# Kernel tuning notes

Hardware: AMD Instinct MI355X
Metric: run time of the kernel (lower is better)

The kernel has to match this reference:

```python
import jax, jax.numpy as jnp
import numpy as np

B, N, C, H, I, ID = 4, 1024, 1024, 16, 77, 768
HD = C // H
HID = 4 * C


def _ln(t, w, b):
    m = jnp.mean(t, axis=-1, keepdims=True)
    v = jnp.mean((t - m) ** 2, axis=-1, keepdims=True)
    return (t - m) * jax.lax.rsqrt(v + 1e-5) * w + b


def _gelu(t):
    return jax.nn.gelu(t, approximate=False)


def setup_inputs() -> dict:
    key = jax.random.key(0)
    ks = iter(jax.random.split(key, 16))

    def nrm(shape, s=0.02):
        return jax.random.normal(next(ks), shape, jnp.float32) * s

    return {
        'x': jax.random.normal(next(ks), (B, N, C), jnp.float32),
        'instruct_states': jax.random.normal(next(ks), (B, I, ID), jnp.float32),
        'norm1_w': jnp.ones((C,), jnp.float32), 'norm1_b': jnp.zeros((C,), jnp.float32),
        'qkv_w': nrm((3 * C, C)),
        'q_bias': jnp.zeros((C,), jnp.float32), 'v_bias': jnp.zeros((C,), jnp.float32),
        'proj_w': nrm((C, C)), 'proj_b': jnp.zeros((C,), jnp.float32),
        'gamma_1': jnp.full((C,), 1e-5, jnp.float32), 'gamma_2': jnp.full((C,), 1e-5, jnp.float32),
        'norm2_w': jnp.ones((C,), jnp.float32), 'norm2_b': jnp.zeros((C,), jnp.float32),
        'fc1_w': nrm((HID, C)), 'fc1_b': jnp.zeros((HID,), jnp.float32),
        'fc2_w': nrm((C, HID)), 'fc2_b': jnp.zeros((C,), jnp.float32),
        'pfc1_w': nrm((HID, C)), 'pfc1_b': jnp.zeros((HID,), jnp.float32),
        'pfc2_w': nrm((C, HID)), 'pfc2_b': jnp.zeros((C,), jnp.float32),
        'parallel_gate': jnp.full((1,), 0.1, jnp.float32),
        'ir_ln_w': jnp.ones((ID,), jnp.float32), 'ir_ln_b': jnp.zeros((ID,), jnp.float32),
        'ir_l1_w': nrm((C, ID)), 'ir_l1_b': jnp.zeros((C,), jnp.float32),
        'ir_l2_w': nrm((C, C)), 'ir_l2_b': jnp.zeros((C,), jnp.float32),
    }


def reference(x, instruct_states, norm1_w, norm1_b, qkv_w, q_bias, v_bias,
              proj_w, proj_b, gamma_1, gamma_2, norm2_w, norm2_b,
              fc1_w, fc1_b, fc2_w, fc2_b, pfc1_w, pfc1_b, pfc2_w, pfc2_b,
              parallel_gate, ir_ln_w, ir_ln_b, ir_l1_w, ir_l1_b, ir_l2_w, ir_l2_b):
    # instruct_dim_reduce: LN -> Linear -> GELU -> Linear
    kv = _ln(instruct_states, ir_ln_w, ir_ln_b)
    kv = _gelu(kv @ ir_l1_w.T + ir_l1_b) @ ir_l2_w.T + ir_l2_b  # [B, I, C]

    xn = _ln(x, norm1_w, norm1_b)                               # [B, N, C]
    cat = jnp.concatenate([kv, xn], axis=1)                     # [B, I+N, C]
    S = I + N

    qkv_bias = jnp.concatenate([q_bias, jnp.zeros_like(v_bias), v_bias])
    qkv = (cat @ qkv_w.T + qkv_bias).reshape(B, S, 3, H, HD)
    q = qkv[:, :, 0].transpose(0, 2, 1, 3)                      # [B, H, S, HD]
    k = qkv[:, :, 1].transpose(0, 2, 1, 3)
    v = qkv[:, :, 2].transpose(0, 2, 1, 3)

    # only visual queries, keys/values over instructions + visual tokens
    q = q[:, :, I:, :] * (HD ** -0.5)                           # [B, H, N, HD]
    attn = jnp.einsum('bhqd,bhkd->bhqk', q, k)                  # [B, H, N, S]
    attn = jax.nn.softmax(attn, axis=-1)
    o = jnp.einsum('bhqk,bhkd->bqhd', attn, v).reshape(B, N, C)
    o = o @ proj_w.T + proj_b

    x = x + gamma_1 * o                                         # LayerScale residual

    y = _ln(x, norm2_w, norm2_b)
    mlp = _gelu(y @ fc1_w.T + fc1_b) @ fc2_w.T + fc2_b
    pmlp = _gelu(y @ pfc1_w.T + pfc1_b) @ pfc2_w.T + pfc2_b
    x = x + gamma_2 * mlp + parallel_gate * pmlp
    return x
```

## Files before the change

kernel.cpp:

```cpp
#include <hip/hip_runtime.h>
#include <cstdint>

#define Bv   4
#define Nv   1024
#define Cv   1024
#define Hv   16
#define Iv   77
#define IDv  768
#define HDv  64
#define HIDv 4096
#define Sv   (Iv + Nv)
#define BIv  (Bv * Iv)
#define BSv  (Bv * Sv)
#define BNv  (Bv * Nv)
#define SPADv 1152

typedef __bf16 bf16x8_t __attribute__((ext_vector_type(8)));
typedef float  f32x4_t  __attribute__((ext_vector_type(4)));
typedef unsigned short us8_t __attribute__((ext_vector_type(8)));
typedef long  l2_t  __attribute__((ext_vector_type(2)));

__device__ inline f32x4_t zero4() { f32x4_t z; z[0]=0.f; z[1]=0.f; z[2]=0.f; z[3]=0.f; return z; }

__device__ inline unsigned short f2bf(float f) {
    unsigned int u = __builtin_bit_cast(unsigned int, f);
    u = (u + 0x7fffu + ((u >> 16) & 1u)) >> 16;
    return (unsigned short)u;
}
__device__ inline float bf2f(unsigned short u) {
    return __builtin_bit_cast(float, ((unsigned int)u) << 16);
}
__device__ inline unsigned int f4_fp8(float a, float b, float c, float d) {
    int v = __builtin_amdgcn_cvt_pk_fp8_f32(a, b, 0, false);
    v = __builtin_amdgcn_cvt_pk_fp8_f32(c, d, v, true);
    return (unsigned int)v;
}

__device__ inline float gelu_f(float x) {
    float u = 0.7978845608f * x * (1.0f + 0.044715f * x * x);
    float e = __expf(2.0f * u);
    float t = 1.0f - 2.0f / (e + 1.0f);
    return 0.5f * x * (1.0f + t);
}

__device__ inline void gload_lds16(const void* g, void* l) {
    __builtin_amdgcn_global_load_lds(
        (__attribute__((address_space(1))) void*)(unsigned long long)g,
        (__attribute__((address_space(3))) void*)(unsigned long long)l,
        16, 0, 0);
}

__global__ __launch_bounds__(256) void cvt8_kernel(
        const float* s0, const float* s1, const float* s2, const float* s3,
        const float* s4, const float* s5, const float* s6, const float* s7,
        void* d0, void* d1, void* d2, void* d3,
        void* d4, void* d5, void* d6, void* d7,
        const float* g1, const float* g2, const float* gate) {
    long i = (long)blockIdx.x * 256 + threadIdx.x;
    const float* src; void* dst; long off;
    const float* sptr = nullptr; int K4 = 1; float wmul = 1.0f; bool f8 = false;
    if (i < 2097152) {
        if (i < 786432)       { src = s0; dst = d0; off = i; }
        else if (i < 1048576) { src = s1; dst = d1; off = i - 786432;  sptr = g1; K4 = 256; }
        else                  { src = s2; dst = d2; off = i - 1048576; f8 = true; wmul = 32.f; }
    } else if (i < 4194304) {
        if (i < 3145728)      { src = s3; dst = d3; off = i - 2097152; f8 = true; wmul = 32.f; sptr = g2; K4 = 1024; }
        else                  { src = s4; dst = d4; off = i - 3145728; f8 = true; wmul = 32.f; }
    } else {
        if (i < 5242880)      { src = s5; dst = d5; off = i - 4194304; f8 = true; wmul = 32.f; sptr = gate; K4 = 0x7fffffff; }
        else if (i < 5439488) { src = s6; dst = d6; off = i - 5242880; }
        else                  { src = s7; dst = d7; off = i - 5439488; }
    }
    float sc = (sptr ? sptr[(int)(off / K4)] : 1.0f) * wmul;
    float4 v = ((const float4*)src)[off];
    if (f8) {
        ((unsigned int*)dst)[off] = f4_fp8(v.x * sc, v.y * sc, v.z * sc, v.w * sc);
    } else {
        ushort4 o = {f2bf(v.x * sc), f2bf(v.y * sc), f2bf(v.z * sc), f2bf(v.w * sc)};
        ((ushort4*)dst)[off] = o;
    }
}

__global__ __launch_bounds__(256) void bias_prep_kernel(
        const float* __restrict__ qb, const float* __restrict__ vb,
        const float* __restrict__ fc2b, const float* __restrict__ pfc2b,
        const float* __restrict__ projb_in,
        const float* __restrict__ fc1b, const float* __restrict__ pfc1b,
        const float* __restrict__ g1, const float* __restrict__ g2,
        const float* __restrict__ gate,
        float* __restrict__ qkvb, float* __restrict__ bfuse,
        float* __restrict__ projb, float* __restrict__ bcat) {
    int i = blockIdx.x * 256 + threadIdx.x;
    if (i < 3 * Cv) {
        float v = 0.f;
        if (i < Cv) v = qb[i];
        else if (i >= 2 * Cv) v = vb[i - 2 * Cv];
        qkvb[i] = v;
    } else if (i < 4 * Cv) {
        int n = i - 3 * Cv;
        bfuse[n] = g2[n] * fc2b[n] + gate[0] * pfc2b[n];
    } else if (i < 5 * Cv) {
        int n = i - 4 * Cv;
        projb[n] = g1[n] * projb_in[n];
    } else if (i < 13 * Cv) {
        int j = i - 5 * Cv;
        bcat[j] = (j < HIDv) ? fc1b[j] : pfc1b[j - HIDv];
    }
}

__global__ __launch_bounds__(256) void scatter_kv_kernel(const unsigned short* __restrict__ kv,
                                                         unsigned short* __restrict__ cat) {
    int r = blockIdx.x;
    int b = r / Iv, i = r % Iv;
    const uint2* src = (const uint2*)(kv + (size_t)r * Cv);
    uint2* dst = (uint2*)(cat + (size_t)(b * Sv + i) * Cv);
    dst[threadIdx.x] = src[threadIdx.x];
}

template <int F8>
__global__ __launch_bounds__(256) void ln_kernel(const float* __restrict__ in,
                                                 const float* __restrict__ w,
                                                 const float* __restrict__ bvec,
                                                 void* __restrict__ out,
                                                 int cols, float invcols,
                                                 int div_, int stride_, int off_) {
    const int r = blockIdx.x;
    const int tid = threadIdx.x;
    const float* row = in + (size_t)r * cols;
    float s = 0.f, s2 = 0.f;
    for (int c = tid * 4; c < cols; c += 1024) {
        float4 v = *(const float4*)(row + c);
        s  += v.x + v.y + v.z + v.w;
        s2 += v.x * v.x + v.y * v.y + v.z * v.z + v.w * v.w;
    }
#pragma unroll
    for (int o2 = 32; o2 > 0; o2 >>= 1) { s += __shfl_down(s, o2); s2 += __shfl_down(s2, o2); }
    __shared__ float sh[10];
    const int lane = tid & 63, wave = tid >> 6;
    if (lane == 0) { sh[wave] = s; sh[4 + wave] = s2; }
    __syncthreads();
    if (tid == 0) {
        float S1 = sh[0] + sh[1] + sh[2] + sh[3];
        float S2 = sh[4] + sh[5] + sh[6] + sh[7];
        float mean = S1 * invcols;
        float var  = S2 * invcols - mean * mean;
        sh[8] = mean;
        sh[9] = rsqrtf(var + 1e-5f);
    }
    __syncthreads();
    const float mean = sh[8], rstd = sh[9];
    const size_t orow = (size_t)((r / div_) * stride_ + (r % div_) + off_) * cols;
    for (int c = tid * 4; c < cols; c += 1024) {
        float4 v  = *(const float4*)(row + c);
        float4 wv = *(const float4*)(w + c);
        float4 bv = *(const float4*)(bvec + c);
        float o0 = (v.x - mean) * rstd * wv.x + bv.x;
        float o1 = (v.y - mean) * rstd * wv.y + bv.y;
        float o2 = (v.z - mean) * rstd * wv.z + bv.z;
        float o3 = (v.w - mean) * rstd * wv.w + bv.w;
        if constexpr (F8) {
            *(unsigned int*)((unsigned char*)out + orow + c) =
                f4_fp8(o0 * 16.f, o1 * 16.f, o2 * 16.f, o3 * 16.f);
        } else {
            ushort4 o = {f2bf(o0), f2bf(o1), f2bf(o2), f2bf(o3)};
            *(ushort4*)((unsigned short*)out + orow + c) = o;
        }
    }
}

template <int MODE>
__global__ __launch_bounds__(256) void gemm_bf16_kernel(
        const unsigned short* __restrict__ A,
        const unsigned short* __restrict__ W,
        const float* __restrict__ bias,
        unsigned short* __restrict__ outp,
        int M, int N, int K) {
    __shared__ unsigned short As[2][128 * 32];
    __shared__ unsigned short Bs[2][128 * 32];
    const int tid  = threadIdx.x;
    const int lane = tid & 63;
    const int wave = tid >> 6;
    const int m16  = lane & 15;
    const int g4   = lane >> 4;
    const int n0 = blockIdx.x * 128;
    const int m0 = blockIdx.y * 128;
    const int wm = (wave >> 1) * 64;
    const int wn = (wave & 1) * 64;

    const int r0  = tid >> 2;
    const int cc0 = (tid & 3) * 8;
    int am0 = m0 + r0;       if (am0 > M - 1) am0 = M - 1;
    int am1 = m0 + r0 + 64;  if (am1 > M - 1) am1 = M - 1;
    const unsigned short* agp0 = A + (size_t)am0 * K + cc0;
    const unsigned short* agp1 = A + (size_t)am1 * K + cc0;
    const unsigned short* bgp0 = W + (size_t)(n0 + r0) * K + cc0;
    const unsigned short* bgp1 = W + (size_t)(n0 + r0 + 64) * K + cc0;

    f32x4_t acc[4][4];
#pragma unroll
    for (int a = 0; a < 4; ++a)
#pragma unroll
        for (int bb = 0; bb < 4; ++bb) acc[a][bb] = zero4();

    auto stage = [&](int buf) {
        gload_lds16(agp0, &As[buf][wave * 512]);
        gload_lds16(agp1, &As[buf][2048 + wave * 512]);
        gload_lds16(bgp0, &Bs[buf][wave * 512]);
        gload_lds16(bgp1, &Bs[buf][2048 + wave * 512]);
        agp0 += 32; agp1 += 32; bgp0 += 32; bgp1 += 32;
    };

    stage(0);
    const int NIT = K >> 5;
    for (int it = 0; it < NIT; ++it) {
        const int cur = it & 1;
        __syncthreads();
        if (it + 1 < NIT) stage(cur ^ 1);
        bf16x8_t xf[4], wf[4];
#pragma unroll
        for (int bb = 0; bb < 4; ++bb)
            xf[bb] = *(const bf16x8_t*)&As[cur][(wm + bb * 16 + m16) * 32 + g4 * 8];
#pragma unroll
        for (int a = 0; a < 4; ++a)
            wf[a] = *(const bf16x8_t*)&Bs[cur][(wn + a * 16 + m16) * 32 + g4 * 8];
#pragma unroll
        for (int a = 0; a < 4; ++a)
#pragma unroll
            for (int bb = 0; bb < 4; ++bb)
                acc[a][bb] = __builtin_amdgcn_mfma_f32_16x16x32_bf16(wf[a], xf[bb], acc[a][bb], 0, 0, 0);
    }

#pragma unroll
    for (int a = 0; a < 4; ++a) {
        const int cb = n0 + wn + a * 16 + g4 * 4;
        const float4 bv4 = *(const float4*)(bias + cb);
#pragma unroll
        for (int bb = 0; bb < 4; ++bb) {
            const int r = m0 + wm + bb * 16 + m16;
            if (r < M) {
                const size_t idx = (size_t)r * N + cb;
                const float v0 = acc[a][bb][0] + bv4.x;
                const float v1 = acc[a][bb][1] + bv4.y;
                const float v2 = acc[a][bb][2] + bv4.z;
                const float v3 = acc[a][bb][3] + bv4.w;
                if constexpr (MODE == 0) {
                    ushort4 o = {f2bf(v0), f2bf(v1), f2bf(v2), f2bf(v3)};
                    *(ushort4*)(outp + idx) = o;
                } else {
                    ushort4 o = {f2bf(gelu_f(v0)), f2bf(gelu_f(v1)),
                                 f2bf(gelu_f(v2)), f2bf(gelu_f(v3))};
                    *(ushort4*)(outp + idx) = o;
                }
            }
        }
    }
}

__global__ __launch_bounds__(256) void gemm_splitk_kernel(
        const unsigned short* __restrict__ A1,
        const unsigned short* __restrict__ W1,
        unsigned short* __restrict__ parts,
        int M, int N, int KA, int Kc) {
    __shared__ unsigned short As[2][128 * 32];
    __shared__ unsigned short Bs[2][128 * 32];
    const int tid  = threadIdx.x;
    const int lane = tid & 63;
    const int wave = tid >> 6;
    const int m16  = lane & 15;
    const int g4   = lane >> 4;
    const int bid = blockIdx.x;
    const int xcd = bid & 7, l = bid >> 3;
    const int by = (xcd << 2) | (l & 3);
    const int rr = l >> 2;
    const int bx = rr & 7;
    const int z  = rr >> 3;
    const int n0 = bx * 128;
    const int m0 = by * 128;
    const int wm = (wave >> 1) * 64;
    const int wn = (wave & 1) * 64;
    const int k0 = z * Kc;

    const int r0  = tid >> 2;
    const int cc0 = (tid & 3) * 8;
    const unsigned short* agp0 = A1 + (size_t)(m0 + r0) * KA + k0 + cc0;
    const unsigned short* agp1 = A1 + (size_t)(m0 + r0 + 64) * KA + k0 + cc0;
    const unsigned short* bgp0 = W1 + (size_t)(n0 + r0) * KA + k0 + cc0;
    const unsigned short* bgp1 = W1 + (size_t)(n0 + r0 + 64) * KA + k0 + cc0;

    f32x4_t acc[4][4];
#pragma unroll
    for (int a = 0; a < 4; ++a)
#pragma unroll
        for (int bb = 0; bb < 4; ++bb) acc[a][bb] = zero4();

    auto stage = [&](int buf) {
        gload_lds16(agp0, &As[buf][wave * 512]);
        gload_lds16(agp1, &As[buf][2048 + wave * 512]);
        gload_lds16(bgp0, &Bs[buf][wave * 512]);
        gload_lds16(bgp1, &Bs[buf][2048 + wave * 512]);
        agp0 += 32; agp1 += 32; bgp0 += 32; bgp1 += 32;
    };

    stage(0);
    const int NIT = Kc >> 5;
    for (int it = 0; it < NIT; ++it) {
        const int cur = it & 1;
        __syncthreads();
        if (it + 1 < NIT) stage(cur ^ 1);
        bf16x8_t xf[4], wf[4];
#pragma unroll
        for (int bb = 0; bb < 4; ++bb)
            xf[bb] = *(const bf16x8_t*)&As[cur][(wm + bb * 16 + m16) * 32 + g4 * 8];
#pragma unroll
        for (int a = 0; a < 4; ++a)
            wf[a] = *(const bf16x8_t*)&Bs[cur][(wn + a * 16 + m16) * 32 + g4 * 8];
#pragma unroll
        for (int a = 0; a < 4; ++a)
#pragma unroll
            for (int bb = 0; bb < 4; ++bb)
                acc[a][bb] = __builtin_amdgcn_mfma_f32_16x16x32_bf16(wf[a], xf[bb], acc[a][bb], 0, 0, 0);
    }

    unsigned short* pz = parts + (size_t)z * M * N;
#pragma unroll
    for (int a = 0; a < 4; ++a) {
        const int cb = n0 + wn + a * 16 + g4 * 4;
#pragma unroll
        for (int bb = 0; bb < 4; ++bb) {
            const int r = m0 + wm + bb * 16 + m16;
            const size_t idx = (size_t)r * N + cb;
            ushort4 o = {f2bf(acc[a][bb][0]), f2bf(acc[a][bb][1]),
                         f2bf(acc[a][bb][2]), f2bf(acc[a][bb][3])};
            *(ushort4*)(pz + idx) = o;
        }
    }
}

__global__ __launch_bounds__(256) void gemm_fp8_gelu_kernel(
        const unsigned char* __restrict__ A,
        const unsigned char* __restrict__ W,
        const float* __restrict__ bias,
        unsigned char* __restrict__ outp,
        int M, int N, int K) {
    __shared__ unsigned char As[2][128 * 64];
    __shared__ unsigned char Bs[2][128 * 64];
    const int tid  = threadIdx.x;
    const int lane = tid & 63;
    const int wave = tid >> 6;
    const int m16  = lane & 15;
    const int g4   = lane >> 4;
    const int bid = blockIdx.x;
    const int xcd = bid & 7, l = bid >> 3;
    const int by = (xcd << 2) | (l & 3);
    const int bx = l >> 2;
    const int n0 = bx * 128;
    const int m0 = by * 128;
    const int wm = (wave >> 1) * 64;
    const int wn = (wave & 1) * 64;

    const int r0  = tid >> 2;
    const int cc0 = (tid & 3) * 16;
    const unsigned char* agp0 = A + (size_t)(m0 + r0) * K + cc0;
    const unsigned char* agp1 = A + (size_t)(m0 + r0 + 64) * K + cc0;
    const unsigned char* bgp0 = W + (size_t)(n0 + r0) * K + cc0;
    const unsigned char* bgp1 = W + (size_t)(n0 + r0 + 64) * K + cc0;

    f32x4_t acc[4][4];
#pragma unroll
    for (int a = 0; a < 4; ++a)
#pragma unroll
        for (int bb = 0; bb < 4; ++bb) acc[a][bb] = zero4();

    auto stage = [&](int buf) {
        gload_lds16(agp0, &As[buf][wave * 1024]);
        gload_lds16(agp1, &As[buf][4096 + wave * 1024]);
        gload_lds16(bgp0, &Bs[buf][wave * 1024]);
        gload_lds16(bgp1, &Bs[buf][4096 + wave * 1024]);
        agp0 += 64; agp1 += 64; bgp0 += 64; bgp1 += 64;
    };

    stage(0);
    const int NIT = K >> 6;
    for (int it = 0; it < NIT; ++it) {
        const int cur = it & 1;
        __syncthreads();
        if (it + 1 < NIT) stage(cur ^ 1);
        l2_t xv[4], wv[4];
#pragma unroll
        for (int bb = 0; bb < 4; ++bb)
            xv[bb] = *(const l2_t*)&As[cur][(wm + bb * 16 + m16) * 64 + g4 * 16];
#pragma unroll
        for (int a = 0; a < 4; ++a)
            wv[a] = *(const l2_t*)&Bs[cur][(wn + a * 16 + m16) * 64 + g4 * 16];
#pragma unroll
        for (int a = 0; a < 4; ++a)
#pragma unroll
            for (int bb = 0; bb < 4; ++bb) {
                acc[a][bb] = __builtin_amdgcn_mfma_f32_16x16x32_fp8_fp8(wv[a][0], xv[bb][0], acc[a][bb], 0, 0, 0);
                acc[a][bb] = __builtin_amdgcn_mfma_f32_16x16x32_fp8_fp8(wv[a][1], xv[bb][1], acc[a][bb], 0, 0, 0);
            }
    }

    const float ds = 1.0f / 512.0f;
#pragma unroll
    for (int a = 0; a < 4; ++a) {
        const int cb = n0 + wn + a * 16 + g4 * 4;
        const float4 bv4 = *(const float4*)(bias + cb);
#pragma unroll
        for (int bb = 0; bb < 4; ++bb) {
            const int r = m0 + wm + bb * 16 + m16;
            const size_t idx = (size_t)r * N + cb;
            unsigned int pk = f4_fp8(gelu_f(acc[a][bb][0] * ds + bv4.x) * 16.f,
                                     gelu_f(acc[a][bb][1] * ds + bv4.y) * 16.f,
                                     gelu_f(acc[a][bb][2] * ds + bv4.z) * 16.f,
                                     gelu_f(acc[a][bb][3] * ds + bv4.w) * 16.f);
            *(unsigned int*)(outp + idx) = pk;
        }
    }
}

__global__ __launch_bounds__(256) void gemm_fp8_splitk_kernel(
        const unsigned char* __restrict__ A1,
        const unsigned char* __restrict__ W1,
        const unsigned char* __restrict__ A2,
        const unsigned char* __restrict__ W2,
        unsigned short* __restrict__ parts,
        int M, int N, int lda, int ldw, int Kc, int zsplit) {
    __shared__ unsigned char As[2][128 * 64];
    __shared__ unsigned char Bs[2][128 * 64];
    const int tid  = threadIdx.x;
    const int lane = tid & 63;
    const int wave = tid >> 6;
    const int m16  = lane & 15;
    const int g4   = lane >> 4;
    const int bid = blockIdx.x;
    const int xcd = bid & 7, l = bid >> 3;
    const int by = (xcd << 2) | (l & 3);
    const int rr = l >> 2;
    const int bx = rr & 7;
    const int z  = rr >> 3;
    const int n0 = bx * 128;
    const int m0 = by * 128;
    const int wm = (wave >> 1) * 64;
    const int wn = (wave & 1) * 64;

    const unsigned char* A = (z < zsplit) ? A1 : A2;
    const unsigned char* W = (z < zsplit) ? W1 : W2;
    const int k0 = (z % zsplit) * Kc;

    const int r0  = tid >> 2;
    const int cc0 = (tid & 3) * 16;
    const unsigned char* agp0 = A + (size_t)(m0 + r0) * lda + k0 + cc0;
    const unsigned char* agp1 = A + (size_t)(m0 + r0 + 64) * lda + k0 + cc0;
    const unsigned char* bgp0 = W + (size_t)(n0 + r0) * ldw + k0 + cc0;
    const unsigned char* bgp1 = W + (size_t)(n0 + r0 + 64) * ldw + k0 + cc0;

    f32x4_t acc[4][4];
#pragma unroll
    for (int a = 0; a < 4; ++a)
#pragma unroll
        for (int bb = 0; bb < 4; ++bb) acc[a][bb] = zero4();

    auto stage = [&](int buf) {
        gload_lds16(agp0, &As[buf][wave * 1024]);
        gload_lds16(agp1, &As[buf][4096 + wave * 1024]);
        gload_lds16(bgp0, &Bs[buf][wave * 1024]);
        gload_lds16(bgp1, &Bs[buf][4096 + wave * 1024]);
        agp0 += 64; agp1 += 64; bgp0 += 64; bgp1 += 64;
    };

    stage(0);
    const int NIT = Kc >> 6;
    for (int it = 0; it < NIT; ++it) {
        const int cur = it & 1;
        __syncthreads();
        if (it + 1 < NIT) stage(cur ^ 1);
        l2_t xv[4], wv[4];
#pragma unroll
        for (int bb = 0; bb < 4; ++bb)
            xv[bb] = *(const l2_t*)&As[cur][(wm + bb * 16 + m16) * 64 + g4 * 16];
#pragma unroll
        for (int a = 0; a < 4; ++a)
            wv[a] = *(const l2_t*)&Bs[cur][(wn + a * 16 + m16) * 64 + g4 * 16];
#pragma unroll
        for (int a = 0; a < 4; ++a)
#pragma unroll
            for (int bb = 0; bb < 4; ++bb) {
                acc[a][bb] = __builtin_amdgcn_mfma_f32_16x16x32_fp8_fp8(wv[a][0], xv[bb][0], acc[a][bb], 0, 0, 0);
                acc[a][bb] = __builtin_amdgcn_mfma_f32_16x16x32_fp8_fp8(wv[a][1], xv[bb][1], acc[a][bb], 0, 0, 0);
            }
    }

    unsigned short* pz = parts + (size_t)z * M * N;
    const float ds = 1.0f / 512.0f;
#pragma unroll
    for (int a = 0; a < 4; ++a) {
        const int cb = n0 + wn + a * 16 + g4 * 4;
#pragma unroll
        for (int bb = 0; bb < 4; ++bb) {
            const int r = m0 + wm + bb * 16 + m16;
            const size_t idx = (size_t)r * N + cb;
            ushort4 o = {f2bf(acc[a][bb][0] * ds), f2bf(acc[a][bb][1] * ds),
                         f2bf(acc[a][bb][2] * ds), f2bf(acc[a][bb][3] * ds)};
            *(ushort4*)(pz + idx) = o;
        }
    }
}

template <int NP>
__global__ __launch_bounds__(256) void reduce_kernel(
        const unsigned short* __restrict__ parts,
        const float* __restrict__ resid,
        const float* __restrict__ bias,
        float* __restrict__ out, int MN, int N4mask) {
    int i = blockIdx.x * 256 + threadIdx.x;
    if (i * 4 >= MN) return;
    float4 res = ((const float4*)resid)[i];
    float4 bv  = *(const float4*)(bias + (i & N4mask) * 4);
    float4 o = {res.x + bv.x, res.y + bv.y, res.z + bv.z, res.w + bv.w};
#pragma unroll
    for (int z = 0; z < NP; ++z) {
        ushort4 u = ((const ushort4*)(parts + (size_t)z * MN))[i];
        o.x += bf2f(u.x); o.y += bf2f(u.y); o.z += bf2f(u.z); o.w += bf2f(u.w);
    }
    ((float4*)out)[i] = o;
}

__global__ __launch_bounds__(256) void vtrans_kernel(const unsigned short* __restrict__ qkv,
                                                     unsigned short* __restrict__ vt) {
    __shared__ unsigned short Vs[64 * 64];
    const int stile = blockIdx.x;
    const int bh = blockIdx.y;
    const int b = bh >> 4, h = bh & 15;
    const int tid = threadIdx.x;
#pragma unroll
    for (int j = 0; j < 2; ++j) {
        int c = j * 256 + tid;
        int r = c >> 3, d8 = (c & 7) * 8;
        int s = stile * 64 + r;
        uint4 v = {0u, 0u, 0u, 0u};
        if (s < Sv) v = *(const uint4*)(qkv + ((size_t)(b * Sv + s) * 3 + 2) * Cv + h * 64 + d8);
        *(uint4*)&Vs[r * 64 + d8] = v;
    }
    __syncthreads();
    const int d  = tid >> 2;
    const int p0 = (tid & 3) * 16;
    unsigned short tmp[16];
#pragma unroll
    for (int e = 0; e < 16; ++e) {
        int p = p0 + e;
        int s_local = (p & 32) + 16 * ((p >> 2) & 1) + 4 * ((p & 31) >> 3) + (p & 3);
        tmp[e] = Vs[s_local * 64 + d];
    }
    unsigned short* dst = vt + ((size_t)bh * 64 + d) * SPADv + stile * 64 + p0;
    *(uint4*)dst       = *(const uint4*)&tmp[0];
    *(uint4*)(dst + 8) = *(const uint4*)&tmp[8];
}

__global__ __launch_bounds__(256) void attn_kernel(const unsigned short* __restrict__ qkv,
                                                   const unsigned short* __restrict__ vt,
                                                   unsigned short* __restrict__ o) {
    __shared__ unsigned short Qs[64 * 64];
    __shared__ unsigned short Ks[2][64 * 64];
    __shared__ unsigned short Vts[2][64 * 64];

    const int tid  = threadIdx.x;
    const int lane = tid & 63;
    const int wave = tid >> 6;
    const int m16  = lane & 15;
    const int g4   = lane >> 4;
    const int qt = blockIdx.x;
    const int bh = blockIdx.y;
    const int b = bh >> 4, h = bh & 15;

    const int lr = lane >> 3;
    const int csw = ((lane & 7) ^ lr) * 8;
    const int sw7 = m16 & 7;

#pragma unroll
    for (int j = 0; j < 2; ++j) {
        int r = wave * 16 + j * 8 + lr;
        int s = Iv + qt * 64 + r;
        gload_lds16(qkv + ((size_t)(b * Sv + s) * 3) * Cv + h * 64 + csw,
                    &Qs[(wave * 16 + j * 8) * 64]);
    }

    auto stage_kv = [&](int st, int buf) {
#pragma unroll
        for (int j = 0; j < 2; ++j) {
            int r = wave * 16 + j * 8 + lr;
            int s = st * 64 + r; if (s > Sv - 1) s = Sv - 1;
            gload_lds16(qkv + ((size_t)(b * Sv + s) * 3 + 1) * Cv + h * 64 + csw,
                        &Ks[buf][(wave * 16 + j * 8) * 64]);
            gload_lds16(vt + ((size_t)bh * 64 + r) * SPADv + st * 64 + csw,
                        &Vts[buf][(wave * 16 + j * 8) * 64]);
        }
    };

    f32x4_t oacc[4];
#pragma unroll
    for (int dt = 0; dt < 4; ++dt) oacc[dt] = zero4();
    float m_run = -1e30f, l_run = 0.f;

    stage_kv(0, 0);
    __syncthreads();

    const bf16x8_t qf0 = *(const bf16x8_t*)&Qs[(wave * 16 + m16) * 64 + ((g4 ^ sw7) * 8)];
    const bf16x8_t qf1 = *(const bf16x8_t*)&Qs[(wave * 16 + m16) * 64 + (((4 + g4) ^ sw7) * 8)];

    const int NT = (Sv + 63) / 64;
    for (int st = 0; st < NT; ++st) {
        const int cur = st & 1;
        if (st + 1 < NT) stage_kv(st + 1, cur ^ 1);

        f32x4_t sc[4];
#pragma unroll
        for (int kt = 0; kt < 4; ++kt) {
            bf16x8_t k0 = *(const bf16x8_t*)&Ks[cur][(kt * 16 + m16) * 64 + ((g4 ^ sw7) * 8)];
            bf16x8_t k1 = *(const bf16x8_t*)&Ks[cur][(kt * 16 + m16) * 64 + (((4 + g4) ^ sw7) * 8)];
            f32x4_t z = zero4();
            z = __builtin_amdgcn_mfma_f32_16x16x32_bf16(k0, qf0, z, 0, 0, 0);
            z = __builtin_amdgcn_mfma_f32_16x16x32_bf16(k1, qf1, z, 0, 0, 0);
            sc[kt] = z;
        }

        float mx = -1e30f;
#pragma unroll
        for (int kt = 0; kt < 4; ++kt)
#pragma unroll
            for (int r = 0; r < 4; ++r) {
                int key = st * 64 + kt * 16 + g4 * 4 + r;
                float v = sc[kt][r] * 0.125f;
                v = (key < Sv) ? v : -1e30f;
                sc[kt][r] = v;
                mx = fmaxf(mx, v);
            }
        mx = fmaxf(mx, __shfl_xor(mx, 16));
        mx = fmaxf(mx, __shfl_xor(mx, 32));
        const float mnew  = fmaxf(m_run, mx);
        const float alpha = __expf(m_run - mnew);
        m_run = mnew;
        float sum = 0.f;
#pragma unroll
        for (int kt = 0; kt < 4; ++kt)
#pragma unroll
            for (int r = 0; r < 4; ++r) {
                float p = __expf(sc[kt][r] - mnew);
                sc[kt][r] = p;
                sum += p;
            }
        sum += __shfl_xor(sum, 16);
        sum += __shfl_xor(sum, 32);
        l_run = l_run * alpha + sum;
#pragma unroll
        for (int dt = 0; dt < 4; ++dt) oacc[dt] *= alpha;

        us8_t pu0, pu1;
#pragma unroll
        for (int j = 0; j < 8; ++j) {
            pu0[j] = f2bf(sc[(j >> 2)][j & 3]);
            pu1[j] = f2bf(sc[2 + (j >> 2)][j & 3]);
        }
        const bf16x8_t pf0 = __builtin_bit_cast(bf16x8_t, pu0);
        const bf16x8_t pf1 = __builtin_bit_cast(bf16x8_t, pu1);

#pragma unroll
        for (int dt = 0; dt < 4; ++dt) {
            bf16x8_t v0 = *(const bf16x8_t*)&Vts[cur][(dt * 16 + m16) * 64 + ((g4 ^ sw7) * 8)];
            bf16x8_t v1 = *(const bf16x8_t*)&Vts[cur][(dt * 16 + m16) * 64 + (((4 + g4) ^ sw7) * 8)];
            oacc[dt] = __builtin_amdgcn_mfma_f32_16x16x32_bf16(v0, pf0, oacc[dt], 0, 0, 0);
            oacc[dt] = __builtin_amdgcn_mfma_f32_16x16x32_bf16(v1, pf1, oacc[dt], 0, 0, 0);
        }
        __syncthreads();
    }

    const float inv = 1.0f / l_run;
    const int q = qt * 64 + wave * 16 + m16;
    const size_t row = (size_t)(b * Nv + q) * Cv + h * 64;
#pragma unroll
    for (int dt = 0; dt < 4; ++dt) {
        ushort4 o4 = {f2bf(oacc[dt][0] * inv), f2bf(oacc[dt][1] * inv),
                      f2bf(oacc[dt][2] * inv), f2bf(oacc[dt][3] * inv)};
        *(ushort4*)&o[row + dt * 16 + g4 * 4] = o4;
    }
}

extern "C" void kernel_launch(void* const* d_in, const int* in_sizes, int n_in,
                              void* d_out, int out_size, void* d_ws, size_t ws_size,
                              hipStream_t stream) {
    (void)in_sizes; (void)n_in; (void)out_size; (void)ws_size;
    const float* x       = (const float*)d_in[0];
    const float* instr   = (const float*)d_in[1];
    const float* norm1_w = (const float*)d_in[2];
    const float* norm1_b = (const float*)d_in[3];
    const float* qkv_w   = (const float*)d_in[4];
    const float* q_bias  = (const float*)d_in[5];
    const float* v_bias  = (const float*)d_in[6];
    const float* proj_w  = (const float*)d_in[7];
    const float* proj_b  = (const float*)d_in[8];
    const float* gamma_1 = (const float*)d_in[9];
    const float* gamma_2 = (const float*)d_in[10];
    const float* norm2_w = (const float*)d_in[11];
    const float* norm2_b = (const float*)d_in[12];
    const float* fc1_w   = (const float*)d_in[13];
    const float* fc1_b   = (const float*)d_in[14];
    const float* fc2_w   = (const float*)d_in[15];
    const float* fc2_b   = (const float*)d_in[16];
    const float* pfc1_w  = (const float*)d_in[17];
    const float* pfc1_b  = (const float*)d_in[18];
    const float* pfc2_w  = (const float*)d_in[19];
    const float* pfc2_b  = (const float*)d_in[20];
    const float* gate    = (const float*)d_in[21];
    const float* ir_ln_w = (const float*)d_in[22];
    const float* ir_ln_b = (const float*)d_in[23];
    const float* ir_l1_w = (const float*)d_in[24];
    const float* ir_l1_b = (const float*)d_in[25];
    const float* ir_l2_w = (const float*)d_in[26];
    const float* ir_l2_b = (const float*)d_in[27];
    float* out = (float*)d_out;

    char* ws = (char*)d_ws;
    size_t off = 0;
    auto alloc = [&](size_t bytes) -> char* {
        char* p = ws + off;
        off += (bytes + 255) & ~(size_t)255;
        return p;
    };
    unsigned short* w_qkv  = (unsigned short*)alloc((size_t)3 * Cv * Cv * 2);
    unsigned short* w_proj = (unsigned short*)alloc((size_t)Cv * Cv * 2);
    unsigned char*  w_mlp1 = (unsigned char*)alloc((size_t)2 * HIDv * Cv);
    unsigned char*  w_fc2  = (unsigned char*)alloc((size_t)Cv * HIDv);
    unsigned char*  w_pfc2 = (unsigned char*)alloc((size_t)Cv * HIDv);
    unsigned short* w_ir1  = (unsigned short*)alloc((size_t)Cv * IDv * 2);
    unsigned short* w_ir2  = (unsigned short*)alloc((size_t)Cv * Cv * 2);
    float*          qkvb   = (float*)alloc((size_t)3 * Cv * 4);
    float*          bfuse  = (float*)alloc((size_t)Cv * 4);
    float*          projb  = (float*)alloc((size_t)Cv * 4);
    float*          bcat   = (float*)alloc((size_t)2 * HIDv * 4);
    unsigned short* irln   = (unsigned short*)alloc((size_t)BIv * IDv * 2);
    unsigned short* h1     = (unsigned short*)alloc((size_t)BIv * Cv * 2);
    unsigned short* kvtmp  = (unsigned short*)alloc((size_t)BIv * Cv * 2);
    unsigned short* cat    = (unsigned short*)alloc((size_t)BSv * Cv * 2);
    unsigned short* qkvbuf = (unsigned short*)alloc((size_t)BSv * 3 * Cv * 2);
    unsigned short* obuf   = (unsigned short*)alloc((size_t)BNv * Cv * 2);
    float*          x1     = (float*)alloc((size_t)BNv * Cv * 4);
    unsigned char*  ybuf8  = (unsigned char*)alloc((size_t)BNv * Cv);
    unsigned char*  gbufA  = (unsigned char*)alloc((size_t)BNv * 2 * HIDv);
    unsigned short* fpart  = (unsigned short*)alloc((size_t)4 * BNv * Cv * 2);
    unsigned short* vt     = (unsigned short*)gbufA;
    unsigned short* ppart  = cat;

    cvt8_kernel<<<22272, 256, 0, stream>>>(qkv_w, proj_w, fc1_w, fc2_w, pfc1_w, pfc2_w,
                                           ir_l1_w, ir_l2_w,
                                           w_qkv, w_proj, w_mlp1, w_fc2,
                                           w_mlp1 + (size_t)HIDv * Cv, w_pfc2,
                                           w_ir1, w_ir2,
                                           gamma_1, gamma_2, gate);

    bias_prep_kernel<<<52, 256, 0, stream>>>(q_bias, v_bias, fc2_b, pfc2_b, proj_b,
                                             fc1_b, pfc1_b,
                                             gamma_1, gamma_2, gate,
                                             qkvb, bfuse, projb, bcat);

    ln_kernel<0><<<BIv, 256, 0, stream>>>(instr, ir_ln_w, ir_ln_b, irln,
                                          IDv, 1.0f / IDv, 1 << 28, 0, 0);
    ln_kernel<0><<<BNv, 256, 0, stream>>>(x, norm1_w, norm1_b, cat,
                                          Cv, 1.0f / Cv, Nv, Sv, Iv);
    gemm_bf16_kernel<1><<<dim3(Cv / 128, (BIv + 127) / 128), 256, 0, stream>>>(
        irln, w_ir1, ir_l1_b, h1, BIv, Cv, IDv);
    gemm_bf16_kernel<0><<<dim3(Cv / 128, (BIv + 127) / 128), 256, 0, stream>>>(
        h1, w_ir2, ir_l2_b, kvtmp, BIv, Cv, Cv);
    scatter_kv_kernel<<<BIv, 256, 0, stream>>>(kvtmp, cat);

    gemm_bf16_kernel<0><<<dim3(3 * Cv / 128, (BSv + 127) / 128), 256, 0, stream>>>(
        cat, w_qkv, qkvb, qkvbuf, BSv, 3 * Cv, Cv);

    vtrans_kernel<<<dim3(18, Bv * Hv), 256, 0, stream>>>(qkvbuf, vt);
    attn_kernel<<<dim3(Nv / 64, Bv * Hv), 256, 0, stream>>>(qkvbuf, vt, obuf);

    gemm_splitk_kernel<<<1024, 256, 0, stream>>>(
        obuf, w_proj, ppart, BNv, Cv, Cv, Cv / 4);
    reduce_kernel<4><<<(BNv * Cv / 4 + 255) / 256, 256, 0, stream>>>(
        ppart, x, projb, x1, BNv * Cv, Cv / 4 - 1);

    ln_kernel<1><<<BNv, 256, 0, stream>>>(x1, norm2_w, norm2_b, ybuf8,
                                          Cv, 1.0f / Cv, 1 << 28, 0, 0);

    gemm_fp8_gelu_kernel<<<2048, 256, 0, stream>>>(
        ybuf8, w_mlp1, bcat, gbufA, BNv, 2 * HIDv, Cv);

    gemm_fp8_splitk_kernel<<<1024, 256, 0, stream>>>(
        gbufA, w_fc2, gbufA + HIDv, w_pfc2, fpart,
        BNv, Cv, 2 * HIDv, HIDv, HIDv / 2, 2);
    reduce_kernel<4><<<(BNv * Cv / 4 + 255) / 256, 256, 0, stream>>>(
        fpart, x1, bfuse, out, BNv * Cv, Cv / 4 - 1);
}
```

Baseline: 505.0 us.

## Use gfx950 16x16x128 scaled FP8 MFMA with K=128 tiles and swizzled LDS

Replaces the pairs of 16x16x32 FP8 MFMAs in the GELU and split-K FP8 GEMMs with the gfx950 16x16x128 f8f6f4 scaled MFMA, using unit scales. The K tile grows from 64 to 128 and LDS buffers double. An XOR swizzle on 16-byte slots keeps LDS fragment reads conflict-free. The aim is fewer MFMA issues and barriers per K step, at the cost of more LDS per block, which may reduce occupancy.

```diff
diff --git a/kernel.cpp b/kernel.cpp
--- a/kernel.cpp
+++ b/kernel.cpp
@@ -19,6 +19,8 @@
 typedef float  f32x4_t  __attribute__((ext_vector_type(4)));
 typedef unsigned short us8_t __attribute__((ext_vector_type(8)));
 typedef long  l2_t  __attribute__((ext_vector_type(2)));
+typedef int   i32x4_t __attribute__((ext_vector_type(4)));
+typedef int   i32x8_t __attribute__((ext_vector_type(8)));
 
 __device__ inline f32x4_t zero4() { f32x4_t z; z[0]=0.f; z[1]=0.f; z[2]=0.f; z[3]=0.f; return z; }
 
@@ -48,6 +50,15 @@
         (__attribute__((address_space(1))) void*)(unsigned long long)g,
         (__attribute__((address_space(3))) void*)(unsigned long long)l,
         16, 0, 0);
+}
+
+__device__ inline i32x8_t frag32(const unsigned char* p0, const unsigned char* p1) {
+    i32x4_t lo = *(const i32x4_t*)p0;
+    i32x4_t hi = *(const i32x4_t*)p1;
+    i32x8_t r;
+    r[0] = lo[0]; r[1] = lo[1]; r[2] = lo[2]; r[3] = lo[3];
+    r[4] = hi[0]; r[5] = hi[1]; r[6] = hi[2]; r[7] = hi[3];
+    return r;
 }
 
 __global__ __launch_bounds__(256) void cvt8_kernel(
@@ -342,8 +353,8 @@
         const float* __restrict__ bias,
         unsigned char* __restrict__ outp,
         int M, int N, int K) {
-    __shared__ unsigned char As[2][128 * 64];
-    __shared__ unsigned char Bs[2][128 * 64];
+    __shared__ unsigned char As[2][128 * 128];
+    __shared__ unsigned char Bs[2][128 * 128];
     const int tid  = threadIdx.x;
     const int lane = tid & 63;
     const int wave = tid >> 6;
@@ -358,12 +369,14 @@
     const int wm = (wave >> 1) * 64;
     const int wn = (wave & 1) * 64;
 
-    const int r0  = tid >> 2;
-    const int cc0 = (tid & 3) * 16;
-    const unsigned char* agp0 = A + (size_t)(m0 + r0) * K + cc0;
-    const unsigned char* agp1 = A + (size_t)(m0 + r0 + 64) * K + cc0;
-    const unsigned char* bgp0 = W + (size_t)(n0 + r0) * K + cc0;
-    const unsigned char* bgp1 = W + (size_t)(n0 + r0 + 64) * K + cc0;
+    const int rowin = tid >> 3;
+    const int sslot = (tid & 7) ^ (rowin & 7);
+    const unsigned char* agp = A + (size_t)(m0 + rowin) * K + sslot * 16;
+    const unsigned char* bgp = W + (size_t)(n0 + rowin) * K + sslot * 16;
+
+    const int sw = m16 & 7;
+    const int ra0 = ((2 * g4) ^ sw) * 16;
+    const int ra1 = ((2 * g4 + 1) ^ sw) * 16;
 
     f32x4_t acc[4][4];
 #pragma unroll
@@ -372,33 +385,37 @@
         for (int bb = 0; bb < 4; ++bb) acc[a][bb] = zero4();
 
     auto stage = [&](int buf) {
-        gload_lds16(agp0, &As[buf][wave * 1024]);
-        gload_lds16(agp1, &As[buf][4096 + wave * 1024]);
-        gload_lds16(bgp0, &Bs[buf][wave * 1024]);
-        gload_lds16(bgp1, &Bs[buf][4096 + wave * 1024]);
-        agp0 += 64; agp1 += 64; bgp0 += 64; bgp1 += 64;
+#pragma unroll
+        for (int j = 0; j < 4; ++j) {
+            gload_lds16(agp + (size_t)j * 32 * K, &As[buf][j * 4096 + wave * 1024]);
+            gload_lds16(bgp + (size_t)j * 32 * K, &Bs[buf][j * 4096 + wave * 1024]);
+        }
+        agp += 128; bgp += 128;
     };
 
     stage(0);
-    const int NIT = K >> 6;
+    const int NIT = K >> 7;
     for (int it = 0; it < NIT; ++it) {
         const int cur = it & 1;
         __syncthreads();
         if (it + 1 < NIT) stage(cur ^ 1);
-        l2_t xv[4], wv[4];
-#pragma unroll
-        for (int bb = 0; bb < 4; ++bb)
-            xv[bb] = *(const l2_t*)&As[cur][(wm + bb * 16 + m16) * 64 + g4 * 16];
+        i32x8_t xv[4], wv[4];
+#pragma unroll
+        for (int bb = 0; bb < 4; ++bb) {
+            const unsigned char* rb = &As[cur][(wm + bb * 16 + m16) * 128];
+            xv[bb] = frag32(rb + ra0, rb + ra1);
+        }
+#pragma unroll
+        for (int a = 0; a < 4; ++a) {
+            const unsigned char* rb = &Bs[cur][(wn + a * 16 + m16) * 128];
+            wv[a] = frag32(rb + ra0, rb + ra1);
+        }
 #pragma unroll
         for (int a = 0; a < 4; ++a)
-            wv[a] = *(const l2_t*)&Bs[cur][(wn + a * 16 + m16) * 64 + g4 * 16];
-#pragma unroll
-        for (int a = 0; a < 4; ++a)
-#pragma unroll
-            for (int bb = 0; bb < 4; ++bb) {
-                acc[a][bb] = __builtin_amdgcn_mfma_f32_16x16x32_fp8_fp8(wv[a][0], xv[bb][0], acc[a][bb], 0, 0, 0);
-                acc[a][bb] = __builtin_amdgcn_mfma_f32_16x16x32_fp8_fp8(wv[a][1], xv[bb][1], acc[a][bb], 0, 0, 0);
-            }
+#pragma unroll
+            for (int bb = 0; bb < 4; ++bb)
+                acc[a][bb] = __builtin_amdgcn_mfma_scale_f32_16x16x128_f8f6f4(
+                    wv[a], xv[bb], acc[a][bb], 0, 0, 0, 0x7f7f7f7f, 0, 0x7f7f7f7f);
     }
 
     const float ds = 1.0f / 512.0f;
@@ -426,8 +443,8 @@
         const unsigned char* __restrict__ W2,
         unsigned short* __restrict__ parts,
         int M, int N, int lda, int ldw, int Kc, int zsplit) {
-    __shared__ unsigned char As[2][128 * 64];
-    __shared__ unsigned char Bs[2][128 * 64];
+    __shared__ unsigned char As[2][128 * 128];
+    __shared__ unsigned char Bs[2][128 * 128];
     const int tid  = threadIdx.x;
     const int lane = tid & 63;
     const int wave = tid >> 6;
@@ -448,12 +465,14 @@
     const unsigned char* W = (z < zsplit) ? W1 : W2;
     const int k0 = (z % zsplit) * Kc;
 
-    const int r0  = tid >> 2;
-    const int cc0 = (tid & 3) * 16;
-    const unsigned char* agp0 = A + (size_t)(m0 + r0) * lda + k0 + cc0;
-    const unsigned char* agp1 = A + (size_t)(m0 + r0 + 64) * lda + k0 + cc0;
-    const unsigned char* bgp0 = W + (size_t)(n0 + r0) * ldw + k0 + cc0;
-    const unsigned char* bgp1 = W + (size_t)(n0 + r0 + 64) * ldw + k0 + cc0;
+    const int rowin = tid >> 3;
+    const int sslot = (tid & 7) ^ (rowin & 7);
+    const unsigned char* agp = A + (size_t)(m0 + rowin) * lda + k0 + sslot * 16;
+    const unsigned char* bgp = W + (size_t)(n0 + rowin) * ldw + k0 + sslot * 16;
+
+    const int sw = m16 & 7;
+    const int ra0 = ((2 * g4) ^ sw) * 16;
+    const int ra1 = ((2 * g4 + 1) ^ sw) * 16;
 
     f32x4_t acc[4][4];
 #pragma unroll
@@ -462,33 +481,37 @@
         for (int bb = 0; bb < 4; ++bb) acc[a][bb] = zero4();
 
     auto stage = [&](int buf) {
-        gload_lds16(agp0, &As[buf][wave * 1024]);
-        gload_lds16(agp1, &As[buf][4096 + wave * 1024]);
-        gload_lds16(bgp0, &Bs[buf][wave * 1024]);
-        gload_lds16(bgp1, &Bs[buf][4096 + wave * 1024]);
-        agp0 += 64; agp1 += 64; bgp0 += 64; bgp1 += 64;
+#pragma unroll
+        for (int j = 0; j < 4; ++j) {
+            gload_lds16(agp + (size_t)j * 32 * lda, &As[buf][j * 4096 + wave * 1024]);
+            gload_lds16(bgp + (size_t)j * 32 * ldw, &Bs[buf][j * 4096 + wave * 1024]);
+        }
+        agp += 128; bgp += 128;
     };
 
     stage(0);
-    const int NIT = Kc >> 6;
+    const int NIT = Kc >> 7;
     for (int it = 0; it < NIT; ++it) {
         const int cur = it & 1;
         __syncthreads();
         if (it + 1 < NIT) stage(cur ^ 1);
-        l2_t xv[4], wv[4];
-#pragma unroll
-        for (int bb = 0; bb < 4; ++bb)
-            xv[bb] = *(const l2_t*)&As[cur][(wm + bb * 16 + m16) * 64 + g4 * 16];
+        i32x8_t xv[4], wv[4];
+#pragma unroll
+        for (int bb = 0; bb < 4; ++bb) {
+            const unsigned char* rb = &As[cur][(wm + bb * 16 + m16) * 128];
+            xv[bb] = frag32(rb + ra0, rb + ra1);
+        }
+#pragma unroll
+        for (int a = 0; a < 4; ++a) {
+            const unsigned char* rb = &Bs[cur][(wn + a * 16 + m16) * 128];
+            wv[a] = frag32(rb + ra0, rb + ra1);
+        }
 #pragma unroll
         for (int a = 0; a < 4; ++a)
-            wv[a] = *(const l2_t*)&Bs[cur][(wn + a * 16 + m16) * 64 + g4 * 16];
-#pragma unroll
-        for (int a = 0; a < 4; ++a)
-#pragma unroll
-            for (int bb = 0; bb < 4; ++bb) {
-                acc[a][bb] = __builtin_amdgcn_mfma_f32_16x16x32_fp8_fp8(wv[a][0], xv[bb][0], acc[a][bb], 0, 0, 0);
-                acc[a][bb] = __builtin_amdgcn_mfma_f32_16x16x32_fp8_fp8(wv[a][1], xv[bb][1], acc[a][bb], 0, 0, 0);
-            }
+#pragma unroll
+            for (int bb = 0; bb < 4; ++bb)
+                acc[a][bb] = __builtin_amdgcn_mfma_scale_f32_16x16x128_f8f6f4(
+                    wv[a], xv[bb], acc[a][bb], 0, 0, 0, 0x7f7f7f7f, 0, 0x7f7f7f7f);
     }
 
     unsigned short* pz = parts + (size_t)z * M * N;
```

Result: faster. 482.4 us (-4.5%).
